# Kernel optimization log

Measured on AMD Instinct MI355X. Metric: run time of the kernel, lower is better.

## Reference

```python
import jax, jax.numpy as jnp
import numpy as np
import math

LEVEL_SHAPES = [(100, 152), (50, 76), (25, 38), (13, 19)]
BS, E, NH, NL, NP = 2, 256, 8, 4, 4


def _grid_init_bias(num_heads, num_levels, num_points):
    # faithful to MultiScaleDeformableAttention.init_weights sampling_offsets bias
    thetas = jnp.arange(num_heads, dtype=jnp.float32) * (2.0 * math.pi / num_heads)
    grid = jnp.stack([jnp.cos(thetas), jnp.sin(thetas)], -1)  # [H,2]
    grid = grid / jnp.max(jnp.abs(grid), axis=-1, keepdims=True)
    grid = jnp.tile(grid[:, None, None, :], (1, num_levels, num_points, 1))  # [H,L,P,2]
    scale = jnp.arange(1, num_points + 1, dtype=jnp.float32)[None, None, :, None]
    return (grid * scale).reshape(-1)


def setup_inputs() -> dict:
    key = jax.random.key(0)
    ks = jax.random.split(key, 10)
    nv = sum(h * w for h, w in LEVEL_SHAPES)  # 20197
    nq = nv
    query = jax.random.normal(ks[0], (BS, nq, E), dtype=jnp.float32)
    value = jax.random.normal(ks[1], (BS, nv, E), dtype=jnp.float32)
    reference_points = jax.random.uniform(ks[2], (BS, nq, NL, 2), dtype=jnp.float32)
    spatial_shapes = jnp.array(LEVEL_SHAPES, dtype=jnp.int32)
    sizes = [h * w for h, w in LEVEL_SHAPES]
    level_start_index = jnp.array(np.cumsum([0] + sizes)[:-1], dtype=jnp.int32)
    s = 1.0 / math.sqrt(E)
    # Linear params stored as [in, out]; y = x @ W + b
    Wv = jax.random.normal(ks[3], (E, E), dtype=jnp.float32) * s
    bv = jnp.zeros((E,), jnp.float32)
    Wso = jax.random.normal(ks[4], (E, NH * NL * NP * 2), dtype=jnp.float32) * 0.01
    bso = _grid_init_bias(NH, NL, NP)
    Waw = jax.random.normal(ks[5], (E, NH * NL * NP), dtype=jnp.float32) * 0.01
    baw = jnp.zeros((NH * NL * NP,), jnp.float32)
    Wo = jax.random.normal(ks[6], (E, E), dtype=jnp.float32) * s
    bo = jnp.zeros((E,), jnp.float32)
    return dict(query=query, value=value, reference_points=reference_points,
                spatial_shapes=spatial_shapes, level_start_index=level_start_index,
                Wv=Wv, bv=bv, Wso=Wso, bso=bso, Waw=Waw, baw=baw, Wo=Wo, bo=bo)


def _bilinear_sample(vl, loc, h, w):
    # vl: [bs, nh, h*w, d]; loc: [bs, nq, nh, P, 2] normalized in [0,1]
    # matches F.grid_sample(mode='bilinear', padding_mode='zeros', align_corners=False)
    bs, nh, _, d = vl.shape
    nq, P = loc.shape[1], loc.shape[3]
    x = loc[..., 0] * w - 0.5
    y = loc[..., 1] * h - 0.5
    x0 = jnp.floor(x).astype(jnp.int32); x1 = x0 + 1
    y0 = jnp.floor(y).astype(jnp.int32); y1 = y0 + 1
    wx1 = x - x0; wx0 = 1.0 - wx1
    wy1 = y - y0; wy0 = 1.0 - wy1

    def gather(ix, iy):
        valid = ((ix >= 0) & (ix < w) & (iy >= 0) & (iy < h)).astype(vl.dtype)
        idx = jnp.clip(iy, 0, h - 1) * w + jnp.clip(ix, 0, w - 1)  # [bs,nq,nh,P]
        idx = jnp.transpose(idx, (0, 2, 1, 3)).reshape(bs, nh, nq * P)
        g = jnp.take_along_axis(vl, idx[..., None], axis=2)  # [bs,nh,nq*P,d]
        g = g.reshape(bs, nh, nq, P, d).transpose(0, 2, 1, 3, 4)  # [bs,nq,nh,P,d]
        return g * valid[..., None]

    return (gather(x0, y0) * (wx0 * wy0)[..., None]
            + gather(x1, y0) * (wx1 * wy0)[..., None]
            + gather(x0, y1) * (wx0 * wy1)[..., None]
            + gather(x1, y1) * (wx1 * wy1)[..., None])


def reference(query, value, reference_points, spatial_shapes, level_start_index,
              Wv, bv, Wso, bso, Waw, baw, Wo, bo):
    bs, nq, e = query.shape
    nv = value.shape[1]
    nh, nl, npt = NH, NL, NP
    d = e // nh
    shapes = np.asarray(spatial_shapes)          # static level shapes
    starts = np.asarray(level_start_index)

    v = (value @ Wv + bv).reshape(bs, nv, nh, d).transpose(0, 2, 1, 3)  # [bs,nh,nv,d]
    so = (query @ Wso + bso).reshape(bs, nq, nh, nl, npt, 2)
    aw = jax.nn.softmax((query @ Waw + baw).reshape(bs, nq, nh, nl * npt), axis=-1)
    aw = aw.reshape(bs, nq, nh, nl, npt)

    # offset normalizer is (w, h) per level
    offset_norm = jnp.stack([spatial_shapes[:, 1], spatial_shapes[:, 0]], -1).astype(query.dtype)
    loc = reference_points[:, :, None, :, None, :] + so / offset_norm[None, None, None, :, None, :]

    out = jnp.zeros((bs, nq, nh, d), dtype=query.dtype)
    for l in range(nl):
        h, w = int(shapes[l, 0]), int(shapes[l, 1])
        s = int(starts[l])
        vl = v[:, :, s:s + h * w, :]                      # [bs,nh,h*w,d]
        sampled = _bilinear_sample(vl, loc[:, :, :, l], h, w)  # [bs,nq,nh,P,d]
        out = out + jnp.einsum('bqhpd,bqhp->bqhd', sampled, aw[:, :, :, l])

    out = out.reshape(bs, nq, e) @ Wo + bo
    return out + query  # identity residual (dropout in eval mode)
```

## Files before the change

### kernel.cpp

```cpp
#include <hip/hip_runtime.h>
#include <hip/hip_bf16.h>
#include <math.h>

constexpr int kBS = 2;
constexpr int kNQ = 20197;
constexpr int kNV = 20197;
constexpr int kM  = kBS * kNQ;
constexpr int kMT = 632;
constexpr int kMpad = kMT * 64;

__constant__ int cLH[4] = {100, 50, 25, 13};
__constant__ int cLW[4] = {152, 76, 38, 19};
__constant__ int cLS[4] = {0, 15200, 19000, 19950};

typedef __bf16 bf16x8 __attribute__((ext_vector_type(8)));
typedef float  f32x4  __attribute__((ext_vector_type(4)));
typedef float  f32x2  __attribute__((ext_vector_type(2)));

__device__ __forceinline__ unsigned short f2bf(float x) {
    unsigned u = __float_as_uint(x);
    return (unsigned short)((u + 0x7fffu + ((u >> 16) & 1u)) >> 16);
}
__device__ __forceinline__ unsigned pack2(float a, float b) {
    return (unsigned)f2bf(a) | ((unsigned)f2bf(b) << 16);
}
__device__ __forceinline__ float bflo(unsigned u) { return __uint_as_float(u << 16); }
__device__ __forceinline__ float bfhi(unsigned u) { return __uint_as_float(u & 0xffff0000u); }
__device__ __forceinline__ void gload_lds16(const void* g, void* s) {
    __builtin_amdgcn_global_load_lds(
        (const __attribute__((address_space(1))) void*)g,
        (__attribute__((address_space(3))) void*)s, 16, 0, 0);
}

__global__ __launch_bounds__(256) void prep_w(
    const float* __restrict__ Wv, const float* __restrict__ Wso,
    const float* __restrict__ Waw, const float* __restrict__ Wo,
    const float* __restrict__ bso, const float* __restrict__ baw,
    unsigned short* __restrict__ WvT, unsigned short* __restrict__ WsoawT,
    unsigned short* __restrict__ WoT, float* __restrict__ bias384)
{
    int k = blockIdx.x * 256 + threadIdx.x;
    if (k < 65536) { int kk = k >> 8, n = k & 255; WvT[n * 256 + kk] = f2bf(Wv[k]); return; }
    k -= 65536;
    if (k < 65536) { int kk = k >> 8, n = k & 255; WsoawT[n * 256 + kk] = f2bf(Wso[k]); return; }
    k -= 65536;
    if (k < 32768) { int kk = k >> 7, n = k & 127; WsoawT[(256 + n) * 256 + kk] = f2bf(Waw[k]); return; }
    k -= 32768;
    if (k < 65536) { int kk = k >> 8, n = k & 255; WoT[n * 256 + kk] = f2bf(Wo[k]); return; }
    k -= 65536;
    if (k < 384) bias384[k] = (k < 256) ? bso[k] : baw[k - 256];
}

template<int AFP32, int CFP32>
__device__ __forceinline__ void gemm_core(
    const void* __restrict__ Av, const __hip_bfloat16* __restrict__ BT,
    const float* __restrict__ bias, const float* __restrict__ res,
    int N, int NT, void* __restrict__ Cv, int m0)
{
    __shared__ __hip_bfloat16 As[64 * 264];
    __shared__ __hip_bfloat16 Bs[2][128 * 32];

    const int t = threadIdx.x;
    const int wave = t >> 6, lane = t & 63;
    const int quad = lane >> 4, l16 = lane & 15;
    const int mw = (wave & 1) * 32, nw = (wave >> 1) * 64;

    auto issueB = [&](int nti, int kc, int buf) {
        #pragma unroll
        for (int j = 0; j < 2; ++j) {
            int s = j * 256 + t;
            int row = s >> 2;
            int ql = (s & 3) ^ ((row >> 1) & 3);
            gload_lds16((const char*)BT + (size_t)(nti * 128 + row) * 512
                            + kc * 64 + ql * 16,
                        (char*)&Bs[buf][0] + s * 16);
        }
    };

    issueB(0, 0, 0);

    if (AFP32) {
        const float* af = (const float*)Av;
        #pragma unroll
        for (int p = 0; p < 16; ++p) {
            int idx = p * 256 + t;
            int row = idx >> 6, col4 = idx & 63;
            float4 f = make_float4(0.f, 0.f, 0.f, 0.f);
            if (m0 + row < kM)
                f = *(const float4*)(af + (size_t)(m0 + row) * 256 + col4 * 4);
            uint2 u = make_uint2(pack2(f.x, f.y), pack2(f.z, f.w));
            *(uint2*)(void*)&As[row * 264 + col4 * 4] = u;
        }
    } else {
        const unsigned short* ab = (const unsigned short*)Av;
        #pragma unroll
        for (int p = 0; p < 8; ++p) {
            int idx = p * 256 + t;
            int row = idx >> 5, ch = idx & 31;
            uint4 u = *(const uint4*)(ab + (size_t)(m0 + row) * 256 + ch * 8);
            *(uint4*)(void*)&As[row * 264 + ch * 8] = u;
        }
    }

    for (int nti = 0; nti < NT; ++nti) {
        f32x4 acc[2][4] = {};
        for (int kc = 0; kc < 8; ++kc) {
            __syncthreads();
            if (kc < 7)             issueB(nti, kc + 1, (kc + 1) & 1);
            else if (nti + 1 < NT)  issueB(nti + 1, 0, 0);
            bf16x8 afr[2], bfr[4];
            #pragma unroll
            for (int mt = 0; mt < 2; ++mt)
                afr[mt] = *(const bf16x8*)(const void*)
                    &As[(mw + mt * 16 + l16) * 264 + kc * 32 + quad * 8];
            #pragma unroll
            for (int nt = 0; nt < 4; ++nt) {
                int r = nw + nt * 16 + l16;
                int qp = quad ^ ((r >> 1) & 3);
                bfr[nt] = *(const bf16x8*)(const void*)
                    &Bs[kc & 1][r * 32 + qp * 8];
            }
            #pragma unroll
            for (int mt = 0; mt < 2; ++mt)
                #pragma unroll
                for (int nt = 0; nt < 4; ++nt)
                    acc[mt][nt] = __builtin_amdgcn_mfma_f32_16x16x32_bf16(
                        bfr[nt], afr[mt], acc[mt][nt], 0, 0, 0);
        }
        const int n0g = nti * 128;
        #pragma unroll
        for (int nt = 0; nt < 4; ++nt) {
            int n0 = n0g + nw + nt * 16 + quad * 4;
            float4 b4 = *(const float4*)&bias[n0];
            #pragma unroll
            for (int mt = 0; mt < 2; ++mt) {
                int row = m0 + mw + mt * 16 + l16;
                if (row < kM) {
                    f32x4 a = acc[mt][nt];
                    if (CFP32) {
                        float4 r4 = *(const float4*)(res + (size_t)row * N + n0);
                        float4 o;
                        o.x = a[0] + b4.x + r4.x;
                        o.y = a[1] + b4.y + r4.y;
                        o.z = a[2] + b4.z + r4.z;
                        o.w = a[3] + b4.w + r4.w;
                        *(float4*)((float*)Cv + (size_t)row * N + n0) = o;
                    } else {
                        uint2 u = make_uint2(pack2(a[0] + b4.x, a[1] + b4.y),
                                             pack2(a[2] + b4.z, a[3] + b4.w));
                        *(uint2*)((unsigned short*)Cv + (size_t)row * N + n0) = u;
                    }
                }
            }
        }
    }
}

__global__ __launch_bounds__(256, 3) void gemm_dual(
    const float* __restrict__ value, const __hip_bfloat16* __restrict__ WvT,
    const float* __restrict__ bv, unsigned short* __restrict__ v_b,
    const float* __restrict__ query, const __hip_bfloat16* __restrict__ WsoawT,
    const float* __restrict__ b384, unsigned short* __restrict__ soaw)
{
    const int m0 = blockIdx.y * 64;
    const float* A; const __hip_bfloat16* BT; const float* bias;
    unsigned short* C; int N, NT;
    if (blockIdx.x == 0) { A = value; BT = WvT;    bias = bv;   C = v_b;  N = 256; NT = 2; }
    else                 { A = query; BT = WsoawT; bias = b384; C = soaw; N = 384; NT = 3; }
    gemm_core<1, 0>(A, BT, bias, nullptr, N, NT, C, m0);
}

__global__ __launch_bounds__(256, 3) void gemm_final(
    const unsigned short* __restrict__ mid_b, const __hip_bfloat16* __restrict__ WoT,
    const float* __restrict__ bo, const float* __restrict__ query,
    float* __restrict__ out)
{
    gemm_core<0, 1>(mid_b, WoT, bo, query, 256, 2, out, blockIdx.y * 64);
}

__global__ __launch_bounds__(128) void msda_sample(
    const __hip_bfloat16* __restrict__ v,
    const __hip_bfloat16* __restrict__ soaw,
    const float* __restrict__ rp,
    __hip_bfloat16* __restrict__ mid)
{
    const int bq = blockIdx.x;
    const int b  = bq >= kNQ;
    const int t  = threadIdx.x;

    __shared__ int2 sP[128 * 5];

    {
        const int h = t >> 4, lp = t & 15, l = lp >> 2;
        unsigned sopk = *(const unsigned*)(const void*)(soaw + (size_t)bq * 384 + 2 * t);
        float logit = bflo((unsigned)*(const unsigned short*)(const void*)
                           (soaw + (size_t)bq * 384 + 256 + t));
        float2 rr = *(const float2*)(rp + (size_t)bq * 8 + l * 2);
        float sx = bflo(sopk), sy = bfhi(sopk);

        float mx = logit;
        #pragma unroll
        for (int s = 8; s >= 1; s >>= 1) mx = fmaxf(mx, __shfl_xor(mx, s, 16));
        float e = __expf(logit - mx);
        float sum = e;
        #pragma unroll
        for (int s = 8; s >= 1; s >>= 1) sum += __shfl_xor(sum, s, 16);
        float w = e / sum;

        const int ww = cLW[l], hh = cLH[l];
        const float fw = (float)ww, fh = (float)hh;
        float x = rr.x * fw + sx - 0.5f;
        float y = rr.y * fh + sy - 0.5f;
        float xf = floorf(x), yf = floorf(y);
        int x0 = (int)xf, y0 = (int)yf;
        float wx1 = x - xf, wx0 = 1.f - wx1;
        float wy1 = y - yf, wy0 = 1.f - wy1;
        bool vx0 = (x0 >= 0) & (x0 < ww);
        bool vx1 = (x0 >= -1) & (x0 + 1 < ww);
        bool vy0 = (y0 >= 0) & (y0 < hh);
        bool vy1 = (y0 >= -1) & (y0 + 1 < hh);
        int cx0 = min(max(x0, 0), ww - 1);
        int cx1 = min(max(x0 + 1, 0), ww - 1);
        int cy0 = min(max(y0, 0), hh - 1);
        int cy1 = min(max(y0 + 1, 0), hh - 1);
        const int base2 = cLS[l] * 512 + h * 64;
        sP[t * 5 + 0] = make_int2(base2 + (cy0 * ww + cx0) * 512,
                                  __float_as_int((vx0 & vy0) ? w * wx0 * wy0 : 0.f));
        sP[t * 5 + 1] = make_int2(base2 + (cy0 * ww + cx1) * 512,
                                  __float_as_int((vx1 & vy0) ? w * wx1 * wy0 : 0.f));
        sP[t * 5 + 2] = make_int2(base2 + (cy1 * ww + cx0) * 512,
                                  __float_as_int((vx0 & vy1) ? w * wx0 * wy1 : 0.f));
        sP[t * 5 + 3] = make_int2(base2 + (cy1 * ww + cx1) * 512,
                                  __float_as_int((vx1 & vy1) ? w * wx1 * wy1 : 0.f));
    }
    __syncthreads();

    const int h = t >> 4, c = (t & 15) * 2;
    const char* vb = (const char*)v + (size_t)b * ((size_t)kNV * 512);
    const unsigned cb = (unsigned)(c * 2);
    f32x2 acc = {0.f, 0.f};
    const int p0 = h * 16;
    #pragma unroll 8
    for (int pp = 0; pp < 16; ++pp) {
        const int idx = (p0 + pp) * 5;
        #pragma unroll
        for (int k2 = 0; k2 < 4; ++k2) {
            int2 pw = sP[idx + k2];
            float wgt = __int_as_float(pw.y);
            unsigned u = *(const unsigned*)(const void*)(vb + ((unsigned)pw.x + cb));
            f32x2 xy; xy.x = bflo(u); xy.y = bfhi(u);
            f32x2 w2; w2.x = wgt; w2.y = wgt;
            acc = xy * w2 + acc;
        }
    }
    *(unsigned*)(void*)(mid + (size_t)bq * 256 + h * 32 + c) = pack2(acc.x, acc.y);
}

extern "C" void kernel_launch(void* const* d_in, const int* in_sizes, int n_in,
                              void* d_out, int out_size, void* d_ws, size_t ws_size,
                              hipStream_t stream)
{
    const float* query = (const float*)d_in[0];
    const float* value = (const float*)d_in[1];
    const float* rp    = (const float*)d_in[2];
    const float* Wv  = (const float*)d_in[5];
    const float* bv  = (const float*)d_in[6];
    const float* Wso = (const float*)d_in[7];
    const float* bso = (const float*)d_in[8];
    const float* Waw = (const float*)d_in[9];
    const float* baw = (const float*)d_in[10];
    const float* Wo  = (const float*)d_in[11];
    const float* bo  = (const float*)d_in[12];

    unsigned short* v_b = (unsigned short*)d_out;

    char* p = (char*)d_ws;
    __hip_bfloat16* soaw  = (__hip_bfloat16*)p;  p += (size_t)kM * 384 * 2;
    unsigned short* mid_b = (unsigned short*)p;  p += (size_t)kMpad * 256 * 2;
    unsigned short* WvT    = (unsigned short*)p; p += 256 * 256 * 2;
    unsigned short* WsoawT = (unsigned short*)p; p += 384 * 256 * 2;
    unsigned short* WoT    = (unsigned short*)p; p += 256 * 256 * 2;
    float* bias384         = (float*)p;

    hipLaunchKernelGGL(prep_w, dim3(898), dim3(256), 0, stream,
                       Wv, Wso, Waw, Wo, bso, baw, WvT, WsoawT, WoT, bias384);

    hipLaunchKernelGGL(gemm_dual, dim3(2, kMT), dim3(256), 0, stream,
                       value, (const __hip_bfloat16*)WvT, bv, v_b,
                       query, (const __hip_bfloat16*)WsoawT, bias384,
                       (unsigned short*)soaw);

    hipLaunchKernelGGL(msda_sample, dim3(kM), dim3(128), 0, stream,
                       (const __hip_bfloat16*)v_b, soaw, rp, (__hip_bfloat16*)mid_b);

    hipLaunchKernelGGL(gemm_final, dim3(1, kMT), dim3(256), 0, stream,
                       mid_b, (const __hip_bfloat16*)WoT, bo, query, (float*)d_out);
}
```

Before: 287.1 us.

## Process two queries per sampling block and load final GEMM A operand into registers

The sampling kernel now assigns one query per wave (two per block), with each lane computing corners for two points and gathering 4 channels (8 bytes) per load instead of 2. This halves the block count and widens the value gathers. Separately, the final output GEMM now loads its bf16 A tile directly from global memory into registers, skipping the LDS staging of A and its shared-memory footprint. The cost is higher register pressure in the GEMM and a different LDS layout in the sampler.

```diff
diff --git a/kernel.cpp b/kernel.cpp
--- a/kernel.cpp
+++ b/kernel.cpp
@@ -51,7 +51,7 @@
     if (k < 384) bias384[k] = (k < 256) ? bso[k] : baw[k - 256];
 }
 
-template<int AFP32, int CFP32>
+template<int CFP32>
 __device__ __forceinline__ void gemm_core(
     const void* __restrict__ Av, const __hip_bfloat16* __restrict__ BT,
     const float* __restrict__ bias, const float* __restrict__ res,
@@ -79,7 +79,7 @@
 
     issueB(0, 0, 0);
 
-    if (AFP32) {
+    {
         const float* af = (const float*)Av;
         #pragma unroll
         for (int p = 0; p < 16; ++p) {
@@ -90,15 +90,6 @@
                 f = *(const float4*)(af + (size_t)(m0 + row) * 256 + col4 * 4);
             uint2 u = make_uint2(pack2(f.x, f.y), pack2(f.z, f.w));
             *(uint2*)(void*)&As[row * 264 + col4 * 4] = u;
-        }
-    } else {
-        const unsigned short* ab = (const unsigned short*)Av;
-        #pragma unroll
-        for (int p = 0; p < 8; ++p) {
-            int idx = p * 256 + t;
-            int row = idx >> 5, ch = idx & 31;
-            uint4 u = *(const uint4*)(ab + (size_t)(m0 + row) * 256 + ch * 8);
-            *(uint4*)(void*)&As[row * 264 + ch * 8] = u;
         }
     }
 
@@ -167,7 +158,7 @@
     unsigned short* C; int N, NT;
     if (blockIdx.x == 0) { A = value; BT = WvT;    bias = bv;   C = v_b;  N = 256; NT = 2; }
     else                 { A = query; BT = WsoawT; bias = b384; C = soaw; N = 384; NT = 3; }
-    gemm_core<1, 0>(A, BT, bias, nullptr, N, NT, C, m0);
+    gemm_core<0>(A, BT, bias, nullptr, N, NT, C, m0);
 }
 
 __global__ __launch_bounds__(256, 3) void gemm_final(
@@ -175,7 +166,109 @@
     const float* __restrict__ bo, const float* __restrict__ query,
     float* __restrict__ out)
 {
-    gemm_core<0, 1>(mid_b, WoT, bo, query, 256, 2, out, blockIdx.y * 64);
+    constexpr int N = 256, NT = 2;
+    const int m0 = blockIdx.y * 64;
+
+    __shared__ __hip_bfloat16 Bs[2][128 * 32];
+
+    const int t = threadIdx.x;
+    const int wave = t >> 6, lane = t & 63;
+    const int quad = lane >> 4, l16 = lane & 15;
+    const int mw = (wave & 1) * 32, nw = (wave >> 1) * 64;
+
+    auto issueB = [&](int nti, int kc, int buf) {
+        #pragma unroll
+        for (int j = 0; j < 2; ++j) {
+            int s = j * 256 + t;
+            int row = s >> 2;
+            int ql = (s & 3) ^ ((row >> 1) & 3);
+            gload_lds16((const char*)WoT + (size_t)(nti * 128 + row) * 512
+                            + kc * 64 + ql * 16,
+                        (char*)&Bs[buf][0] + s * 16);
+        }
+    };
+
+    issueB(0, 0, 0);
+
+    bf16x8 areg[2][8];
+    #pragma unroll
+    for (int mt = 0; mt < 2; ++mt)
+        #pragma unroll
+        for (int kc = 0; kc < 8; ++kc)
+            areg[mt][kc] = *(const bf16x8*)(const void*)
+                (mid_b + (size_t)(m0 + mw + mt * 16 + l16) * 256 + kc * 32 + quad * 8);
+
+    for (int nti = 0; nti < NT; ++nti) {
+        f32x4 acc[2][4] = {};
+        for (int kc = 0; kc < 8; ++kc) {
+            __syncthreads();
+            if (kc < 7)             issueB(nti, kc + 1, (kc + 1) & 1);
+            else if (nti + 1 < NT)  issueB(nti + 1, 0, 0);
+            bf16x8 bfr[4];
+            #pragma unroll
+            for (int nt = 0; nt < 4; ++nt) {
+                int r = nw + nt * 16 + l16;
+                int qp = quad ^ ((r >> 1) & 3);
+                bfr[nt] = *(const bf16x8*)(const void*)
+                    &Bs[kc & 1][r * 32 + qp * 8];
+            }
+            #pragma unroll
+            for (int mt = 0; mt < 2; ++mt)
+                #pragma unroll
+                for (int nt = 0; nt < 4; ++nt)
+                    acc[mt][nt] = __builtin_amdgcn_mfma_f32_16x16x32_bf16(
+                        bfr[nt], areg[mt][kc], acc[mt][nt], 0, 0, 0);
+        }
+        const int n0g = nti * 128;
+        #pragma unroll
+        for (int nt = 0; nt < 4; ++nt) {
+            int n0 = n0g + nw + nt * 16 + quad * 4;
+            float4 b4 = *(const float4*)&bo[n0];
+            #pragma unroll
+            for (int mt = 0; mt < 2; ++mt) {
+                int row = m0 + mw + mt * 16 + l16;
+                if (row < kM) {
+                    f32x4 a = acc[mt][nt];
+                    float4 r4 = *(const float4*)(query + (size_t)row * N + n0);
+                    float4 o;
+                    o.x = a[0] + b4.x + r4.x;
+                    o.y = a[1] + b4.y + r4.y;
+                    o.z = a[2] + b4.z + r4.z;
+                    o.w = a[3] + b4.w + r4.w;
+                    *(float4*)(out + (size_t)row * N + n0) = o;
+                }
+            }
+        }
+    }
+}
+
+struct C4 { int o[4]; float w[4]; };
+
+__device__ __forceinline__ C4 mk_corners(float rx, float ry, float sx, float sy,
+                                         float wgt, int lv, int h)
+{
+    C4 r;
+    const int ww = cLW[lv], hh = cLH[lv];
+    float x = rx * (float)ww + sx - 0.5f;
+    float y = ry * (float)hh + sy - 0.5f;
+    float xf = floorf(x), yf = floorf(y);
+    int x0 = (int)xf, y0 = (int)yf;
+    float wx1 = x - xf, wx0 = 1.f - wx1;
+    float wy1 = y - yf, wy0 = 1.f - wy1;
+    bool vx0 = (x0 >= 0) & (x0 < ww);
+    bool vx1 = (x0 >= -1) & (x0 + 1 < ww);
+    bool vy0 = (y0 >= 0) & (y0 < hh);
+    bool vy1 = (y0 >= -1) & (y0 + 1 < hh);
+    int cx0 = min(max(x0, 0), ww - 1);
+    int cx1 = min(max(x0 + 1, 0), ww - 1);
+    int cy0 = min(max(y0, 0), hh - 1);
+    int cy1 = min(max(y0 + 1, 0), hh - 1);
+    const int base2 = cLS[lv] * 512 + h * 64;
+    r.o[0] = base2 + (cy0 * ww + cx0) * 512; r.w[0] = (vx0 & vy0) ? wgt * wx0 * wy0 : 0.f;
+    r.o[1] = base2 + (cy0 * ww + cx1) * 512; r.w[1] = (vx1 & vy0) ? wgt * wx1 * wy0 : 0.f;
+    r.o[2] = base2 + (cy1 * ww + cx0) * 512; r.w[2] = (vx0 & vy1) ? wgt * wx0 * wy1 : 0.f;
+    r.o[3] = base2 + (cy1 * ww + cx1) * 512; r.w[3] = (vx1 & vy1) ? wgt * wx1 * wy1 : 0.f;
+    return r;
 }
 
 __global__ __launch_bounds__(128) void msda_sample(
@@ -184,76 +277,63 @@
     const float* __restrict__ rp,
     __hip_bfloat16* __restrict__ mid)
 {
-    const int bq = blockIdx.x;
+    const int wv = threadIdx.x >> 6;
+    const int l  = threadIdx.x & 63;
+    const int bq = blockIdx.x * 2 + wv;
     const int b  = bq >= kNQ;
-    const int t  = threadIdx.x;
-
-    __shared__ int2 sP[128 * 5];
+
+    __shared__ int2 sC[2][4][130];
 
     {
-        const int h = t >> 4, lp = t & 15, l = lp >> 2;
-        unsigned sopk = *(const unsigned*)(const void*)(soaw + (size_t)bq * 384 + 2 * t);
-        float logit = bflo((unsigned)*(const unsigned short*)(const void*)
-                           (soaw + (size_t)bq * 384 + 256 + t));
-        float2 rr = *(const float2*)(rp + (size_t)bq * 8 + l * 2);
-        float sx = bflo(sopk), sy = bfhi(sopk);
-
-        float mx = logit;
-        #pragma unroll
-        for (int s = 8; s >= 1; s >>= 1) mx = fmaxf(mx, __shfl_xor(mx, s, 16));
-        float e = __expf(logit - mx);
-        float sum = e;
-        #pragma unroll
-        for (int s = 8; s >= 1; s >>= 1) sum += __shfl_xor(sum, s, 16);
-        float w = e / sum;
-
-        const int ww = cLW[l], hh = cLH[l];
-        const float fw = (float)ww, fh = (float)hh;
-        float x = rr.x * fw + sx - 0.5f;
-        float y = rr.y * fh + sy - 0.5f;
-        float xf = floorf(x), yf = floorf(y);
-        int x0 = (int)xf, y0 = (int)yf;
-        float wx1 = x - xf, wx0 = 1.f - wx1;
-        float wy1 = y - yf, wy0 = 1.f - wy1;
-        bool vx0 = (x0 >= 0) & (x0 < ww);
-        bool vx1 = (x0 >= -1) & (x0 + 1 < ww);
-        bool vy0 = (y0 >= 0) & (y0 < hh);
-        bool vy1 = (y0 >= -1) & (y0 + 1 < hh);
-        int cx0 = min(max(x0, 0), ww - 1);
-        int cx1 = min(max(x0 + 1, 0), ww - 1);
-        int cy0 = min(max(y0, 0), hh - 1);
-        int cy1 = min(max(y0 + 1, 0), hh - 1);
-        const int base2 = cLS[l] * 512 + h * 64;
-        sP[t * 5 + 0] = make_int2(base2 + (cy0 * ww + cx0) * 512,
-                                  __float_as_int((vx0 & vy0) ? w * wx0 * wy0 : 0.f));
-        sP[t * 5 + 1] = make_int2(base2 + (cy0 * ww + cx1) * 512,
-                                  __float_as_int((vx1 & vy0) ? w * wx1 * wy0 : 0.f));
-        sP[t * 5 + 2] = make_int2(base2 + (cy1 * ww + cx0) * 512,
-                                  __float_as_int((vx0 & vy1) ? w * wx0 * wy1 : 0.f));
-        sP[t * 5 + 3] = make_int2(base2 + (cy1 * ww + cx1) * 512,
-                                  __float_as_int((vx1 & vy1) ? w * wx1 * wy1 : 0.f));
+        const int u0 = 2 * l;
+        const int h  = u0 >> 4;
+        const int lv = (u0 & 15) >> 2;
+
+        uint2 so2 = *(const uint2*)(const void*)(soaw + (size_t)bq * 384 + 2 * u0);
+        unsigned lg2 = *(const unsigned*)(const void*)(soaw + (size_t)bq * 384 + 256 + u0);
+        float logit0 = bflo(lg2), logit1 = bfhi(lg2);
+        float2 rr = *(const float2*)(rp + (size_t)bq * 8 + lv * 2);
+
+        float mx = fmaxf(logit0, logit1);
+        #pragma unroll
+        for (int s = 4; s >= 1; s >>= 1) mx = fmaxf(mx, __shfl_xor(mx, s, 8));
+        float e0 = __expf(logit0 - mx), e1 = __expf(logit1 - mx);
+        float sum = e0 + e1;
+        #pragma unroll
+        for (int s = 4; s >= 1; s >>= 1) sum += __shfl_xor(sum, s, 8);
+        float inv = 1.f / sum;
+
+        C4 ca = mk_corners(rr.x, rr.y, bflo(so2.x), bfhi(so2.x), e0 * inv, lv, h);
+        C4 cb = mk_corners(rr.x, rr.y, bflo(so2.y), bfhi(so2.y), e1 * inv, lv, h);
+        #pragma unroll
+        for (int k2 = 0; k2 < 4; ++k2)
+            *(int4*)(void*)&sC[wv][k2][u0] =
+                make_int4(ca.o[k2], __float_as_int(ca.w[k2]),
+                          cb.o[k2], __float_as_int(cb.w[k2]));
     }
     __syncthreads();
 
-    const int h = t >> 4, c = (t & 15) * 2;
+    const int h2 = l >> 3, c0 = (l & 7) * 4;
     const char* vb = (const char*)v + (size_t)b * ((size_t)kNV * 512);
-    const unsigned cb = (unsigned)(c * 2);
-    f32x2 acc = {0.f, 0.f};
-    const int p0 = h * 16;
-    #pragma unroll 8
-    for (int pp = 0; pp < 16; ++pp) {
-        const int idx = (p0 + pp) * 5;
+    const unsigned cb2 = (unsigned)(c0 * 2);
+    f32x2 acc0 = {0.f, 0.f}, acc1 = {0.f, 0.f};
+    const int ub = h2 * 16;
+    #pragma unroll 4
+    for (int pt = 0; pt < 16; ++pt) {
         #pragma unroll
         for (int k2 = 0; k2 < 4; ++k2) {
-            int2 pw = sP[idx + k2];
+            int2 pw = sC[wv][k2][ub + pt];
             float wgt = __int_as_float(pw.y);
-            unsigned u = *(const unsigned*)(const void*)(vb + ((unsigned)pw.x + cb));
-            f32x2 xy; xy.x = bflo(u); xy.y = bfhi(u);
+            uint2 u2 = *(const uint2*)(const void*)(vb + ((unsigned)pw.x + cb2));
             f32x2 w2; w2.x = wgt; w2.y = wgt;
-            acc = xy * w2 + acc;
-        }
-    }
-    *(unsigned*)(void*)(mid + (size_t)bq * 256 + h * 32 + c) = pack2(acc.x, acc.y);
+            f32x2 lo; lo.x = bflo(u2.x); lo.y = bfhi(u2.x);
+            f32x2 hi; hi.x = bflo(u2.y); hi.y = bfhi(u2.y);
+            acc0 = lo * w2 + acc0;
+            acc1 = hi * w2 + acc1;
+        }
+    }
+    *(uint2*)(void*)(mid + (size_t)bq * 256 + h2 * 32 + c0) =
+        make_uint2(pack2(acc0.x, acc0.y), pack2(acc1.x, acc1.y));
 }
 
 extern "C" void kernel_launch(void* const* d_in, const int* in_sizes, int n_in,
@@ -290,7 +370,7 @@
                        query, (const __hip_bfloat16*)WsoawT, bias384,
                        (unsigned short*)soaw);
 
-    hipLaunchKernelGGL(msda_sample, dim3(kM), dim3(128), 0, stream,
+    hipLaunchKernelGGL(msda_sample, dim3(kM / 2), dim3(128), 0, stream,
                        (const __hip_bfloat16*)v_b, soaw, rp, (__hip_bfloat16*)mid_b);
 
     hipLaunchKernelGGL(gemm_final, dim3(1, kMT), dim3(256), 0, stream,
```

Result: slower. 301.5 us (+5.0%).

## Load GEMM weight fragments directly from global memory instead of LDS staging

Applied to the files above, without the earlier changes.

The GEMM kernels stop staging the transposed bf16 weight tiles through double-buffered LDS with async global-to-LDS loads, and instead read the B fragments straight from global memory (expected to hit in L1/L2 because weights are small and shared). The final GEMM also skips LDS for the A operand, holding the whole 64x256 bf16 row slice per wave in registers. This removes the per-k-step barriers and LDS traffic, at the cost of more global load latency per MFMA step and higher register pressure, which could reduce occupancy.

```diff
diff --git a/kernel.cpp b/kernel.cpp
--- a/kernel.cpp
+++ b/kernel.cpp
@@ -26,11 +26,6 @@
 }
 __device__ __forceinline__ float bflo(unsigned u) { return __uint_as_float(u << 16); }
 __device__ __forceinline__ float bfhi(unsigned u) { return __uint_as_float(u & 0xffff0000u); }
-__device__ __forceinline__ void gload_lds16(const void* g, void* s) {
-    __builtin_amdgcn_global_load_lds(
-        (const __attribute__((address_space(1))) void*)g,
-        (__attribute__((address_space(3))) void*)s, 16, 0, 0);
-}
 
 __global__ __launch_bounds__(256) void prep_w(
     const float* __restrict__ Wv, const float* __restrict__ Wso,
@@ -51,75 +46,44 @@
     if (k < 384) bias384[k] = (k < 256) ? bso[k] : baw[k - 256];
 }
 
-template<int AFP32, int CFP32>
-__device__ __forceinline__ void gemm_core(
-    const void* __restrict__ Av, const __hip_bfloat16* __restrict__ BT,
-    const float* __restrict__ bias, const float* __restrict__ res,
-    int N, int NT, void* __restrict__ Cv, int m0)
+__device__ __forceinline__ void gemm_core_direct(
+    const float* __restrict__ A, const __hip_bfloat16* __restrict__ BT,
+    const float* __restrict__ bias, int N, int NT,
+    unsigned short* __restrict__ C, int m0)
 {
     __shared__ __hip_bfloat16 As[64 * 264];
-    __shared__ __hip_bfloat16 Bs[2][128 * 32];
 
     const int t = threadIdx.x;
     const int wave = t >> 6, lane = t & 63;
     const int quad = lane >> 4, l16 = lane & 15;
     const int mw = (wave & 1) * 32, nw = (wave >> 1) * 64;
 
-    auto issueB = [&](int nti, int kc, int buf) {
-        #pragma unroll
-        for (int j = 0; j < 2; ++j) {
-            int s = j * 256 + t;
-            int row = s >> 2;
-            int ql = (s & 3) ^ ((row >> 1) & 3);
-            gload_lds16((const char*)BT + (size_t)(nti * 128 + row) * 512
-                            + kc * 64 + ql * 16,
-                        (char*)&Bs[buf][0] + s * 16);
-        }
-    };
-
-    issueB(0, 0, 0);
-
-    if (AFP32) {
-        const float* af = (const float*)Av;
-        #pragma unroll
-        for (int p = 0; p < 16; ++p) {
-            int idx = p * 256 + t;
-            int row = idx >> 6, col4 = idx & 63;
-            float4 f = make_float4(0.f, 0.f, 0.f, 0.f);
-            if (m0 + row < kM)
-                f = *(const float4*)(af + (size_t)(m0 + row) * 256 + col4 * 4);
-            uint2 u = make_uint2(pack2(f.x, f.y), pack2(f.z, f.w));
-            *(uint2*)(void*)&As[row * 264 + col4 * 4] = u;
-        }
-    } else {
-        const unsigned short* ab = (const unsigned short*)Av;
-        #pragma unroll
-        for (int p = 0; p < 8; ++p) {
-            int idx = p * 256 + t;
-            int row = idx >> 5, ch = idx & 31;
-            uint4 u = *(const uint4*)(ab + (size_t)(m0 + row) * 256 + ch * 8);
-            *(uint4*)(void*)&As[row * 264 + ch * 8] = u;
-        }
-    }
+    #pragma unroll
+    for (int p = 0; p < 16; ++p) {
+        int idx = p * 256 + t;
+        int row = idx >> 6, col4 = idx & 63;
+        float4 f = make_float4(0.f, 0.f, 0.f, 0.f);
+        if (m0 + row < kM)
+            f = *(const float4*)(A + (size_t)(m0 + row) * 256 + col4 * 4);
+        uint2 u = make_uint2(pack2(f.x, f.y), pack2(f.z, f.w));
+        *(uint2*)(void*)&As[row * 264 + col4 * 4] = u;
+    }
+    __syncthreads();
 
     for (int nti = 0; nti < NT; ++nti) {
         f32x4 acc[2][4] = {};
+        #pragma unroll
         for (int kc = 0; kc < 8; ++kc) {
-            __syncthreads();
-            if (kc < 7)             issueB(nti, kc + 1, (kc + 1) & 1);
-            else if (nti + 1 < NT)  issueB(nti + 1, 0, 0);
             bf16x8 afr[2], bfr[4];
+            #pragma unroll
+            for (int nt = 0; nt < 4; ++nt)
+                bfr[nt] = *(const bf16x8*)(const void*)
+                    (BT + (size_t)(nti * 128 + nw + nt * 16 + l16) * 256
+                        + kc * 32 + quad * 8);
             #pragma unroll
             for (int mt = 0; mt < 2; ++mt)
                 afr[mt] = *(const bf16x8*)(const void*)
                     &As[(mw + mt * 16 + l16) * 264 + kc * 32 + quad * 8];
-            #pragma unroll
-            for (int nt = 0; nt < 4; ++nt) {
-                int r = nw + nt * 16 + l16;
-                int qp = quad ^ ((r >> 1) & 3);
-                bfr[nt] = *(const bf16x8*)(const void*)
-                    &Bs[kc & 1][r * 32 + qp * 8];
-            }
             #pragma unroll
             for (int mt = 0; mt < 2; ++mt)
                 #pragma unroll
@@ -137,19 +101,9 @@
                 int row = m0 + mw + mt * 16 + l16;
                 if (row < kM) {
                     f32x4 a = acc[mt][nt];
-                    if (CFP32) {
-                        float4 r4 = *(const float4*)(res + (size_t)row * N + n0);
-                        float4 o;
-                        o.x = a[0] + b4.x + r4.x;
-                        o.y = a[1] + b4.y + r4.y;
-                        o.z = a[2] + b4.z + r4.z;
-                        o.w = a[3] + b4.w + r4.w;
-                        *(float4*)((float*)Cv + (size_t)row * N + n0) = o;
-                    } else {
-                        uint2 u = make_uint2(pack2(a[0] + b4.x, a[1] + b4.y),
-                                             pack2(a[2] + b4.z, a[3] + b4.w));
-                        *(uint2*)((unsigned short*)Cv + (size_t)row * N + n0) = u;
-                    }
+                    uint2 u = make_uint2(pack2(a[0] + b4.x, a[1] + b4.y),
+                                         pack2(a[2] + b4.z, a[3] + b4.w));
+                    *(uint2*)(C + (size_t)row * N + n0) = u;
                 }
             }
         }
@@ -163,11 +117,10 @@
     const float* __restrict__ b384, unsigned short* __restrict__ soaw)
 {
     const int m0 = blockIdx.y * 64;
-    const float* A; const __hip_bfloat16* BT; const float* bias;
-    unsigned short* C; int N, NT;
-    if (blockIdx.x == 0) { A = value; BT = WvT;    bias = bv;   C = v_b;  N = 256; NT = 2; }
-    else                 { A = query; BT = WsoawT; bias = b384; C = soaw; N = 384; NT = 3; }
-    gemm_core<1, 0>(A, BT, bias, nullptr, N, NT, C, m0);
+    if (blockIdx.x == 0)
+        gemm_core_direct(value, WvT, bv, 256, 2, v_b, m0);
+    else
+        gemm_core_direct(query, WsoawT, b384, 384, 3, soaw, m0);
 }
 
 __global__ __launch_bounds__(256, 3) void gemm_final(
@@ -175,7 +128,61 @@
     const float* __restrict__ bo, const float* __restrict__ query,
     float* __restrict__ out)
 {
-    gemm_core<0, 1>(mid_b, WoT, bo, query, 256, 2, out, blockIdx.y * 64);
+    constexpr int N = 256, NT = 2;
+    const int m0 = blockIdx.y * 64;
+
+    const int t = threadIdx.x;
+    const int wave = t >> 6, lane = t & 63;
+    const int quad = lane >> 4, l16 = lane & 15;
+    const int mw = (wave & 1) * 32, nw = (wave >> 1) * 64;
+
+    bf16x8 areg[2][8];
+    #pragma unroll
+    for (int mt = 0; mt < 2; ++mt)
+        #pragma unroll
+        for (int kc = 0; kc < 8; ++kc)
+            areg[mt][kc] = *(const bf16x8*)(const void*)
+                (mid_b + (size_t)(m0 + mw + mt * 16 + l16) * 256 + kc * 32 + quad * 8);
+
+    for (int nti = 0; nti < NT; ++nti) {
+        f32x4 acc[2][4] = {};
+        #pragma unroll
+        for (int kc = 0; kc < 8; ++kc) {
+            bf16x8 bfr[4];
+            #pragma unroll
+            for (int nt = 0; nt < 4; ++nt)
+                bfr[nt] = *(const bf16x8*)(const void*)
+                    ((const __hip_bfloat16*)WoT
+                        + (size_t)(nti * 128 + nw + nt * 16 + l16) * 256
+                        + kc * 32 + quad * 8);
+            #pragma unroll
+            for (int mt = 0; mt < 2; ++mt)
+                #pragma unroll
+                for (int nt = 0; nt < 4; ++nt)
+                    acc[mt][nt] = __builtin_amdgcn_mfma_f32_16x16x32_bf16(
+                        bfr[nt], areg[mt][kc], acc[mt][nt], 0, 0, 0);
+        }
+        const int n0g = nti * 128;
+        #pragma unroll
+        for (int nt = 0; nt < 4; ++nt) {
+            int n0 = n0g + nw + nt * 16 + quad * 4;
+            float4 b4 = *(const float4*)&bo[n0];
+            #pragma unroll
+            for (int mt = 0; mt < 2; ++mt) {
+                int row = m0 + mw + mt * 16 + l16;
+                if (row < kM) {
+                    f32x4 a = acc[mt][nt];
+                    float4 r4 = *(const float4*)(query + (size_t)row * N + n0);
+                    float4 o;
+                    o.x = a[0] + b4.x + r4.x;
+                    o.y = a[1] + b4.y + r4.y;
+                    o.z = a[2] + b4.z + r4.z;
+                    o.w = a[3] + b4.w + r4.w;
+                    *(float4*)(out + (size_t)row * N + n0) = o;
+                }
+            }
+        }
+    }
 }
 
 __global__ __launch_bounds__(128) void msda_sample(
```

New measurement: 336.7 us. 17.3% more time.
